# Optimization experiments

Hardware: AMD Instinct MI355X
Metric: run time of the kernel (lower is better)

Reference implementation:

```python
import jax, jax.numpy as jnp
import numpy as np

N_HEADS = 16


def setup_inputs() -> dict:
    key = jax.random.key(0)
    ks = jax.random.split(key, 4)
    B, S, E = 4, 2048, 1024
    x = jax.random.normal(ks[0], (B, S, E), dtype=jnp.float32)
    w_attn = jax.random.normal(ks[1], (E, 3 * E), dtype=jnp.float32) * 0.02
    b_attn = jnp.zeros((3 * E,), dtype=jnp.float32)
    w_proj = jax.random.normal(ks[2], (E, E), dtype=jnp.float32) * 0.02
    b_proj = jnp.zeros((E,), dtype=jnp.float32)
    return {"x": x, "w_attn": w_attn, "b_attn": b_attn, "w_proj": w_proj, "b_proj": b_proj}


def reference(x, w_attn, b_attn, w_proj, b_proj):
    B, S, E = x.shape
    H = N_HEADS
    D = E // H
    # fused QKV projection (Conv1D: x @ W + b)
    qkv = x @ w_attn + b_attn                     # [B, S, 3E]
    q, k, v = jnp.split(qkv, 3, axis=-1)          # each [B, S, E]
    q = q.reshape(B, S, H, D).transpose(0, 2, 1, 3)  # [B, H, S, D]
    k = k.reshape(B, S, H, D).transpose(0, 2, 1, 3)
    v = v.reshape(B, S, H, D).transpose(0, 2, 1, 3)
    # scaled QK^T
    scores = jnp.einsum('bhqd,bhkd->bhqk', q, k) / jnp.sqrt(jnp.asarray(D, dtype=x.dtype))
    # causal mask via where with dtype-min fill (matches torch.where(c_m, w, finfo.min))
    causal = jnp.tril(jnp.ones((S, S), dtype=bool))  # [S, S]
    scores = jnp.where(causal[None, None, :, :], scores, jnp.finfo(scores.dtype).min)
    attn = jax.nn.softmax(scores, axis=-1)        # [B, H, S, S]
    o = jnp.einsum('bhqk,bhkd->bhqd', attn, v)    # [B, H, S, D]
    o = o.transpose(0, 2, 1, 3).reshape(B, S, E)  # merge heads
    return o @ w_proj + b_proj                    # output projection
```

## Files before the change

kernel.cpp:

```cpp
#include <hip/hip_runtime.h>
#include <stdint.h>


typedef __bf16 bf16;
typedef __bf16 bf16x4 __attribute__((ext_vector_type(4)));
typedef __bf16 bf16x8 __attribute__((ext_vector_type(8)));
typedef float  f32x4  __attribute__((ext_vector_type(4)));

#define DEV __device__ __forceinline__

DEV void async_copy16(bf16* lds, const bf16* g) {
  __builtin_amdgcn_global_load_lds(
      (__attribute__((address_space(1))) void*)(uintptr_t)g,
      (__attribute__((address_space(3))) void*)(uint32_t)(uintptr_t)lds,
      16, 0, 0);
}

__global__ __launch_bounds__(256) void cast_x_kernel(const float* __restrict__ in,
                                                     bf16* __restrict__ out, int n4) {
  int i = blockIdx.x * blockDim.x + threadIdx.x;
  int stride = gridDim.x * blockDim.x;
  for (; i < n4; i += stride) {
    float4 v = ((const float4*)in)[i];
    bf16x4 o = { (bf16)v.x, (bf16)v.y, (bf16)v.z, (bf16)v.w };
    *(bf16x4*)(out + (size_t)i * 4) = o;
  }
}

__global__ __launch_bounds__(256) void transpose_cast_kernel(const float* __restrict__ W,
                                                             bf16* __restrict__ Wt,
                                                             int Kd, int Nd) {
  __shared__ alignas(16) bf16 T[64 * 80];
  const int t = threadIdx.x;
  const int n0 = blockIdx.x * 64;
  const int k0 = blockIdx.y * 64;
#pragma unroll
  for (int i = 0; i < 4; ++i) {
    int idx = t + i * 256;
    int r  = idx >> 4;
    int c4 = (idx & 15) * 4;
    float4 v = *(const float4*)(W + (size_t)(k0 + r) * Nd + n0 + c4);
    bf16x4 o = { (bf16)v.x, (bf16)v.y, (bf16)v.z, (bf16)v.w };
    *(bf16x4*)(&T[r * 80 + c4]) = o;
  }
  __syncthreads();
#pragma unroll
  for (int i = 0; i < 2; ++i) {
    int idx = t + i * 256;
    int n = idx >> 3;
    int c = idx & 7;
    bf16x8 o;
#pragma unroll
    for (int j = 0; j < 8; ++j) o[j] = T[(c * 8 + j) * 80 + n];
    *(bf16x8*)(Wt + (size_t)(n0 + n) * Kd + k0 + c * 8) = o;
  }
}

__global__ __launch_bounds__(256) void vtrans_kernel(const bf16* __restrict__ qkv,
                                                     bf16* __restrict__ vt) {
  __shared__ alignas(16) bf16 T[64 * 80];
  const int t  = threadIdx.x;
  const int s0 = blockIdx.x * 64;
  const int bh = blockIdx.y;
  const int b = bh >> 4, h = bh & 15;
#pragma unroll
  for (int i = 0; i < 2; ++i) {
    int idx = t + i * 256;
    int s = idx >> 3, c = idx & 7;
    bf16x8 v = *(const bf16x8*)(qkv + (size_t)(b * 2048 + s0 + s) * 3072 + 2048 + h * 64 + c * 8);
    *(bf16x8*)(&T[s * 80 + c * 8]) = v;
  }
  __syncthreads();
#pragma unroll
  for (int i = 0; i < 2; ++i) {
    int idx = t + i * 256;
    int d = idx >> 3, c = idx & 7;
    bf16x8 o;
#pragma unroll
    for (int j = 0; j < 8; ++j) o[j] = T[(c * 8 + j) * 80 + d];
    *(bf16x8*)(vt + (size_t)(bh * 64 + d) * 2048 + s0 + c * 8) = o;
  }
}

template <typename OutT>
__global__ __launch_bounds__(512, 2) void gemm256_kernel(const bf16* __restrict__ A,
                                                         const bf16* __restrict__ Bt,
                                                         const float* __restrict__ bias,
                                                         OutT* __restrict__ C,
                                                         int M, int N, int K,
                                                         float qscale, int qcols,
                                                         int nbx) {
  __shared__ alignas(16) bf16 As[2][256 * 64];
  __shared__ alignas(16) bf16 Bs[2][128 * 64];

  const int tid  = threadIdx.x;
  const int lane = tid & 63;
  const int w    = tid >> 6;
  const int wm = w >> 1, wn = w & 1;
  const int l15 = lane & 15, l16 = lane >> 4;

  const int nwg = (int)gridDim.x;
  const int cpx = nwg >> 3;
  const int swz = ((int)blockIdx.x & 7) * cpx + ((int)blockIdx.x >> 3);
  const int m0 = (swz / nbx) * 256;
  const int n0 = (swz % nbx) * 128;

  const int srow = tid >> 3;
  const int sc   = tid & 7;
#define STAGE_TILE(buf, kt)                                                     \
  {                                                                             \
    const int k0_ = (kt) * 64;                                                  \
    _Pragma("unroll")                                                           \
    for (int j = 0; j < 4; ++j) {                                               \
      int row = j * 64 + srow;                                                  \
      const bf16* src = A + (size_t)(m0 + row) * K + k0_ + 8 * (sc ^ (row & 7));\
      async_copy16(&As[buf][(j * 512 + w * 64) * 8], src);                      \
    }                                                                           \
    _Pragma("unroll")                                                           \
    for (int j = 0; j < 2; ++j) {                                               \
      int row = j * 64 + srow;                                                  \
      const bf16* src = Bt + (size_t)(n0 + row) * K + k0_ + 8 * (sc ^ (row & 7));\
      async_copy16(&Bs[buf][(j * 512 + w * 64) * 8], src);                      \
    }                                                                           \
  }

  f32x4 acc[4][4];
  f32x4 zf = {0.f, 0.f, 0.f, 0.f};
#pragma unroll
  for (int i = 0; i < 4; ++i)
#pragma unroll
    for (int j = 0; j < 4; ++j) acc[i][j] = zf;

  const int KT = K >> 6;
  STAGE_TILE(0, 0)
  STAGE_TILE(1, 1)

#define COMPUTE_TILE(buf)                                                       \
  {                                                                             \
    bf16x8 bfr[4][2];                                                           \
    _Pragma("unroll")                                                           \
    for (int n = 0; n < 4; ++n) {                                               \
      int rb = wn * 64 + n * 16 + l15;                                          \
      _Pragma("unroll")                                                         \
      for (int kk = 0; kk < 2; ++kk)                                            \
        bfr[n][kk] = *(const bf16x8*)(&Bs[buf][rb * 64 + 8 * ((kk * 4 + l16) ^ (rb & 7))]); \
    }                                                                           \
    __builtin_amdgcn_s_setprio(1);                                              \
    _Pragma("unroll")                                                           \
    for (int m = 0; m < 4; ++m) {                                               \
      int ra = wm * 64 + m * 16 + l15;                                          \
      bf16x8 a0 = *(const bf16x8*)(&As[buf][ra * 64 + 8 * ((0 + l16) ^ (ra & 7))]); \
      bf16x8 a1 = *(const bf16x8*)(&As[buf][ra * 64 + 8 * ((4 + l16) ^ (ra & 7))]); \
      _Pragma("unroll")                                                         \
      for (int n = 0; n < 4; ++n)                                               \
        acc[m][n] = __builtin_amdgcn_mfma_f32_16x16x32_bf16(a0, bfr[n][0], acc[m][n], 0, 0, 0); \
      _Pragma("unroll")                                                         \
      for (int n = 0; n < 4; ++n)                                               \
        acc[m][n] = __builtin_amdgcn_mfma_f32_16x16x32_bf16(a1, bfr[n][1], acc[m][n], 0, 0, 0); \
    }                                                                           \
    __builtin_amdgcn_s_setprio(0);                                              \
  }

  for (int kt = 0; kt < KT - 1; ++kt) {
    asm volatile("s_waitcnt vmcnt(6)" ::: "memory");
    __builtin_amdgcn_s_barrier();
    asm volatile("" ::: "memory");
    const int buf = kt & 1;
    COMPUTE_TILE(buf)
    asm volatile("" ::: "memory");
    __builtin_amdgcn_s_barrier();
    if (kt + 2 < KT) STAGE_TILE(buf, kt + 2)
  }
  asm volatile("s_waitcnt vmcnt(0)" ::: "memory");
  __builtin_amdgcn_s_barrier();
  asm volatile("" ::: "memory");
  COMPUTE_TILE((KT - 1) & 1)

#pragma unroll
  for (int n = 0; n < 4; ++n) {
    int col = n0 + wn * 64 + n * 16 + l15;
    float bb = bias[col];
    float sc2 = (col < qcols) ? qscale : 1.0f;
#pragma unroll
    for (int m = 0; m < 4; ++m) {
#pragma unroll
      for (int reg = 0; reg < 4; ++reg) {
        int row = m0 + wm * 64 + m * 16 + l16 * 4 + reg;
        C[(size_t)row * N + col] = (OutT)((acc[m][n][reg] + bb) * sc2);
      }
    }
  }
#undef STAGE_TILE
#undef COMPUTE_TILE
}

__global__ __launch_bounds__(512, 4) void flash_kernel(const bf16* __restrict__ qkv,
                                                       const bf16* __restrict__ vt,
                                                       bf16* __restrict__ obuf) {
  constexpr int S = 2048, E3 = 3072;
  __shared__ alignas(16) bf16 Ks[2][64 * 64];
  __shared__ alignas(16) bf16 Vs[2][64 * 64];
  __shared__ alignas(16) bf16 Ps[8][16 * 64];

  const int tid  = threadIdx.x;
  const int lane = tid & 63;
  const int w    = tid >> 6;
  const int bx = blockIdx.x;
  const int bh = blockIdx.y;
  const int b = bh >> 4, h = bh & 15;
  const int l15 = lane & 15, l16 = lane >> 4;

  const int sr  = w * 8 + (lane >> 3);
  const int scc = lane & 7;
  const bf16* kstage = qkv + (size_t)(b * S + sr) * E3 + 1024 + h * 64 + 8 * (scc ^ (sr & 7));
  const bf16* vstage = vt + (size_t)(bh * 64 + sr) * S + 8 * (scc ^ (sr & 7));

  const int xsw = l15 & 7;
  const uint32_t rdA = (uint32_t)(l15 * 128 + 16 * (l16 ^ xsw));
  const uint32_t rdB = (uint32_t)(l15 * 128 + 16 * ((4 + l16) ^ xsw));
  const uint32_t wbase = (uint32_t)(w * 2048);
  uint32_t pwo[4];
#pragma unroll
  for (int kf = 0; kf < 4; ++kf)
    pwo[kf] = wbase + (uint32_t)(l15 * 128 + (((kf * 2) | (l16 >> 1)) ^ xsw) * 16 + (l16 & 1) * 8);
  const uint32_t pr0 = wbase + rdA, pr1 = wbase + rdB;

#define KV_STAGE(buf, kv0_)                                        \
  {                                                                \
    async_copy16(Ks[buf] + w * 512, kstage + (size_t)(kv0_) * E3); \
    async_copy16(Vs[buf] + w * 512, vstage + (kv0_));              \
  }

  for (int half = 0; half < 2; ++half) {
    const int t = half ? (15 - bx) : bx;
    const int q0 = t * 128;
    const int wq0 = q0 + w * 16;
    const int nsteps = 2 * t + 2;

    KV_STAGE(0, 0)

    bf16x8 qf[2];
    {
      const bf16* qbase = qkv + (size_t)(b * S + wq0 + l15) * E3 + h * 64;
#pragma unroll
      for (int dk = 0; dk < 2; ++dk)
        qf[dk] = *(const bf16x8*)(qbase + (dk * 4 + l16) * 8);
    }

    float lstate = 0.f;
    f32x4 oacc[4];
    f32x4 zf = {0.f, 0.f, 0.f, 0.f};
#pragma unroll
    for (int i = 0; i < 4; ++i) oacc[i] = zf;

    __syncthreads();

#define FLASH_STEP(CUR, STEPIDX)                                                  \
    {                                                                             \
      const int kv0 = (STEPIDX) * 64;                                             \
      if ((STEPIDX) + 1 < nsteps) KV_STAGE((CUR) ^ 1, kv0 + 64)                   \
      if (kv0 <= wq0 + 15) {                     \
        f32x4 sv[4];                                                              \
        _Pragma("unroll")                                                         \
        for (int kf = 0; kf < 4; ++kf) sv[kf] = zf;                               \
        __builtin_amdgcn_s_setprio(1);                                            \
        _Pragma("unroll")                                                         \
        for (int kf = 0; kf < 4; ++kf) {                                          \
          bf16x8 k0 = *(const bf16x8*)((const char*)Ks[CUR] + rdA + kf * 2048);   \
          sv[kf] = __builtin_amdgcn_mfma_f32_16x16x32_bf16(k0, qf[0], sv[kf], 0, 0, 0); \
          bf16x8 k1 = *(const bf16x8*)((const char*)Ks[CUR] + rdB + kf * 2048);   \
          sv[kf] = __builtin_amdgcn_mfma_f32_16x16x32_bf16(k1, qf[1], sv[kf], 0, 0, 0); \
        }                                                                         \
        __builtin_amdgcn_s_setprio(0);                                            \
        if (kv0 + 63 > wq0) {     \
          const int qrow_ = wq0 + l15;                                            \
          _Pragma("unroll")                                                       \
          for (int kf = 0; kf < 4; ++kf)                                          \
            _Pragma("unroll")                                                     \
            for (int reg = 0; reg < 4; ++reg) {                                   \
              int key = kv0 + kf * 16 + l16 * 4 + reg;                            \
              if (key > qrow_) sv[kf][reg] = -1e30f;                              \
            }                                                                     \
        }                                                                         \
        float rsum = 0.f;                                                         \
        _Pragma("unroll")                                                         \
        for (int kf = 0; kf < 4; ++kf) {                                          \
          _Pragma("unroll")                                                       \
          for (int reg = 0; reg < 4; ++reg) {                                     \
            float p = __builtin_amdgcn_exp2f(sv[kf][reg]);                        \
            sv[kf][reg] = p;                                                      \
            rsum += p;                                                            \
          }                                                                       \
          bf16x4 quad = { (bf16)sv[kf][0], (bf16)sv[kf][1],                       \
                          (bf16)sv[kf][2], (bf16)sv[kf][3] };                     \
          *(bf16x4*)((char*)Ps + pwo[kf]) = quad;                                 \
        }                                                                         \
        rsum += __shfl_xor(rsum, 16);                                             \
        rsum += __shfl_xor(rsum, 32);                                             \
        lstate += rsum;                                                           \
        bf16x8 pb0 = *(const bf16x8*)((const char*)Ps + pr0);                     \
        bf16x8 pb1 = *(const bf16x8*)((const char*)Ps + pr1);                     \
        __builtin_amdgcn_s_setprio(1);                                            \
        _Pragma("unroll")                                                         \
        for (int nf = 0; nf < 4; ++nf) {                                          \
          bf16x8 vf0 = *(const bf16x8*)((const char*)Vs[CUR] + rdA + nf * 2048);  \
          oacc[nf] = __builtin_amdgcn_mfma_f32_16x16x32_bf16(vf0, pb0, oacc[nf], 0, 0, 0); \
          bf16x8 vf1 = *(const bf16x8*)((const char*)Vs[CUR] + rdB + nf * 2048);  \
          oacc[nf] = __builtin_amdgcn_mfma_f32_16x16x32_bf16(vf1, pb1, oacc[nf], 0, 0, 0); \
        }                                                                         \
        __builtin_amdgcn_s_setprio(0);                                            \
      }                                                                           \
      __syncthreads();          \
    }

    for (int step = 0; step < nsteps; step += 2) {
      FLASH_STEP(0, step)
      FLASH_STEP(1, step + 1)
    }
#undef FLASH_STEP

    float inv = 1.0f / lstate;
    int qrow = wq0 + l15;
#pragma unroll
    for (int nf = 0; nf < 4; ++nf) {
      bf16x4 o4 = { (bf16)(oacc[nf][0] * inv), (bf16)(oacc[nf][1] * inv),
                    (bf16)(oacc[nf][2] * inv), (bf16)(oacc[nf][3] * inv) };
      *(bf16x4*)(obuf + (size_t)(b * S + qrow) * 1024 + h * 64 + nf * 16 + l16 * 4) = o4;
    }
  }
#undef KV_STAGE
}

extern "C" void kernel_launch(void* const* d_in, const int* in_sizes, int n_in,
                              void* d_out, int out_size, void* d_ws, size_t ws_size,
                              hipStream_t stream) {
  (void)in_sizes; (void)n_in; (void)out_size; (void)ws_size;
  const float* x      = (const float*)d_in[0];
  const float* w_attn = (const float*)d_in[1];
  const float* b_attn = (const float*)d_in[2];
  const float* w_proj = (const float*)d_in[3];
  const float* b_proj = (const float*)d_in[4];
  float* out = (float*)d_out;

  char* ws = (char*)d_ws;
  bf16* xb  = (bf16*)(ws + 0);
  bf16* wat = (bf16*)(ws + 16777216);
  bf16* wpt = (bf16*)(ws + 23068672);
  bf16* qkv = (bf16*)(ws + 25165824);
  bf16* vt  = (bf16*)(ws + 75497472);
  bf16* ob  = (bf16*)(ws + 92274688);

  const float QSCALE = 0.18033688011112042f;

  cast_x_kernel<<<2048, 256, 0, stream>>>(x, xb, 8192 * 1024 / 4);
  transpose_cast_kernel<<<dim3(48, 16), 256, 0, stream>>>(w_attn, wat, 1024, 3072);
  transpose_cast_kernel<<<dim3(16, 16), 256, 0, stream>>>(w_proj, wpt, 1024, 1024);
  gemm256_kernel<bf16><<<768, 512, 0, stream>>>(xb, wat, b_attn, qkv,
                                                8192, 3072, 1024, QSCALE, 1024, 24);
  vtrans_kernel<<<dim3(32, 64), 256, 0, stream>>>(qkv, vt);
  flash_kernel<<<dim3(8, 64), 512, 0, stream>>>(qkv, vt, ob);
  gemm256_kernel<float><<<256, 512, 0, stream>>>(ob, wpt, b_proj, out,
                                                 8192, 1024, 1024, 1.0f, 0, 8);
}
```

Baseline: 168.3 us.

## Triple-buffer GEMM LDS tiles and interleave half-tile staging with MFMA halves

```diff
diff --git a/kernel.cpp b/kernel.cpp
--- a/kernel.cpp
+++ b/kernel.cpp
@@ -90,8 +90,8 @@
                                                          int M, int N, int K,
                                                          float qscale, int qcols,
                                                          int nbx) {
-  __shared__ alignas(16) bf16 As[2][256 * 64];
-  __shared__ alignas(16) bf16 Bs[2][128 * 64];
+  __shared__ alignas(16) bf16 As[3][256 * 64];
+  __shared__ alignas(16) bf16 Bs[3][128 * 64];
 
   const int tid  = threadIdx.x;
   const int lane = tid & 63;
@@ -107,20 +107,19 @@
 
   const int srow = tid >> 3;
   const int sc   = tid & 7;
-#define STAGE_TILE(buf, kt)                                                     \
+#define STAGE_HALF(buf, kt, H)                                                  \
   {                                                                             \
     const int k0_ = (kt) * 64;                                                  \
     _Pragma("unroll")                                                           \
-    for (int j = 0; j < 4; ++j) {                                               \
+    for (int j = 2 * (H); j < 2 * (H) + 2; ++j) {                               \
       int row = j * 64 + srow;                                                  \
       const bf16* src = A + (size_t)(m0 + row) * K + k0_ + 8 * (sc ^ (row & 7));\
       async_copy16(&As[buf][(j * 512 + w * 64) * 8], src);                      \
     }                                                                           \
-    _Pragma("unroll")                                                           \
-    for (int j = 0; j < 2; ++j) {                                               \
-      int row = j * 64 + srow;                                                  \
+    {                                                                           \
+      int row = (H) * 64 + srow;                                                \
       const bf16* src = Bt + (size_t)(n0 + row) * K + k0_ + 8 * (sc ^ (row & 7));\
-      async_copy16(&Bs[buf][(j * 512 + w * 64) * 8], src);                      \
+      async_copy16(&Bs[buf][((H) * 512 + w * 64) * 8], src);                    \
     }                                                                           \
   }
 
@@ -132,22 +131,14 @@
     for (int j = 0; j < 4; ++j) acc[i][j] = zf;
 
   const int KT = K >> 6;
-  STAGE_TILE(0, 0)
-  STAGE_TILE(1, 1)
-
-#define COMPUTE_TILE(buf)                                                       \
+  STAGE_HALF(0, 0, 0) STAGE_HALF(0, 0, 1)
+  STAGE_HALF(1, 1, 0) STAGE_HALF(1, 1, 1)
+
+#define MFMA_HALF(buf, MLO)                                                     \
   {                                                                             \
-    bf16x8 bfr[4][2];                                                           \
-    _Pragma("unroll")                                                           \
-    for (int n = 0; n < 4; ++n) {                                               \
-      int rb = wn * 64 + n * 16 + l15;                                          \
-      _Pragma("unroll")                                                         \
-      for (int kk = 0; kk < 2; ++kk)                                            \
-        bfr[n][kk] = *(const bf16x8*)(&Bs[buf][rb * 64 + 8 * ((kk * 4 + l16) ^ (rb & 7))]); \
-    }                                                                           \
     __builtin_amdgcn_s_setprio(1);                                              \
     _Pragma("unroll")                                                           \
-    for (int m = 0; m < 4; ++m) {                                               \
+    for (int m = (MLO); m < (MLO) + 2; ++m) {                                   \
       int ra = wm * 64 + m * 16 + l15;                                          \
       bf16x8 a0 = *(const bf16x8*)(&As[buf][ra * 64 + 8 * ((0 + l16) ^ (ra & 7))]); \
       bf16x8 a1 = *(const bf16x8*)(&As[buf][ra * 64 + 8 * ((4 + l16) ^ (ra & 7))]); \
@@ -161,20 +152,47 @@
     __builtin_amdgcn_s_setprio(0);                                              \
   }
 
+  int bufc = 0;
+  int bufs = 2;
   for (int kt = 0; kt < KT - 1; ++kt) {
     asm volatile("s_waitcnt vmcnt(6)" ::: "memory");
     __builtin_amdgcn_s_barrier();
     asm volatile("" ::: "memory");
-    const int buf = kt & 1;
-    COMPUTE_TILE(buf)
+    const bool st = (kt + 2 < KT);
+    if (st) STAGE_HALF(bufs, kt + 2, 0)
+    bf16x8 bfr[4][2];
+#pragma unroll
+    for (int n = 0; n < 4; ++n) {
+      int rb = wn * 64 + n * 16 + l15;
+#pragma unroll
+      for (int kk = 0; kk < 2; ++kk)
+        bfr[n][kk] = *(const bf16x8*)(&Bs[bufc][rb * 64 + 8 * ((kk * 4 + l16) ^ (rb & 7))]);
+    }
+    MFMA_HALF(bufc, 0)
     asm volatile("" ::: "memory");
     __builtin_amdgcn_s_barrier();
-    if (kt + 2 < KT) STAGE_TILE(buf, kt + 2)
+    asm volatile("" ::: "memory");
+    if (st) STAGE_HALF(bufs, kt + 2, 1)
+    MFMA_HALF(bufc, 2)
+    asm volatile("" ::: "memory");
+    bufc = (bufc == 2) ? 0 : bufc + 1;
+    bufs = (bufs == 2) ? 0 : bufs + 1;
   }
   asm volatile("s_waitcnt vmcnt(0)" ::: "memory");
   __builtin_amdgcn_s_barrier();
   asm volatile("" ::: "memory");
-  COMPUTE_TILE((KT - 1) & 1)
+  {
+    bf16x8 bfr[4][2];
+#pragma unroll
+    for (int n = 0; n < 4; ++n) {
+      int rb = wn * 64 + n * 16 + l15;
+#pragma unroll
+      for (int kk = 0; kk < 2; ++kk)
+        bfr[n][kk] = *(const bf16x8*)(&Bs[bufc][rb * 64 + 8 * ((kk * 4 + l16) ^ (rb & 7))]);
+    }
+    MFMA_HALF(bufc, 0)
+    MFMA_HALF(bufc, 2)
+  }
 
 #pragma unroll
   for (int n = 0; n < 4; ++n) {
@@ -190,8 +208,8 @@
       }
     }
   }
-#undef STAGE_TILE
-#undef COMPUTE_TILE
+#undef STAGE_HALF
+#undef MFMA_HALF
 }
 
 __global__ __launch_bounds__(512, 4) void flash_kernel(const bf16* __restrict__ qkv,
```

New measurement: 169.8 us. No clear change (+0.9%).
